# Performance work log

Hardware: AMD Instinct MI355X
Metric: run time of the kernel (lower is better)

Reference implementation:

```python
import jax, jax.numpy as jnp
import numpy as np
from jax import lax


def setup_inputs() -> dict:
    key = jax.random.key(0)
    k1, k2, k3 = jax.random.split(key, 3)
    H = W = 2048
    K, p = 16, 15
    x = jax.random.uniform(k1, (1, 1, H, W), dtype=jnp.float32)
    patterns = jax.random.uniform(k2, (K, p, p), dtype=jnp.float32)
    vectors = jax.random.normal(k3, (K, 2), dtype=jnp.float32)
    return {"x": x, "patterns": patterns, "vectors": vectors}


def reference(x, patterns, vectors):
    K, p, _ = patterns.shape
    img = x[0, 0]                      # [H, W]
    H, W = img.shape
    # GENEO_1: pad by p on all sides; window at (i,j) covers padded [i:i+p, j:j+p]
    padded = jnp.pad(img, p)           # [H+2p, W+2p]
    ones_k = jnp.ones((1, 1, p, p), dtype=img.dtype)
    win_sum = lax.conv_general_dilated(
        padded[None, None], ones_k, window_strides=(1, 1), padding='VALID'
    )[0, 0]                            # [H+p+1, W+p+1]
    win_sum = win_sum[:H, :W]          # windows for i in [0,H), j in [0,W)
    # out[k,i,j] = 1 - (sum(pattern_k) - win_sum)/(p*p)
    pat_sum = patterns.sum(axis=(1, 2))                     # [K]
    F_k = 1.0 - (pat_sum[:, None, None] - win_sum[None]) / (p * p)  # [K,H,W]
    # GENEO_3: gather at (i - floor(vx), j - floor(vy)), torch negative-index wrap -> mod
    off = jnp.floor(vectors).astype(jnp.int32)              # [K,2]
    ri = (jnp.arange(H)[None, :] - off[:, 0:1]) % H          # [K,H]
    rj = (jnp.arange(W)[None, :] - off[:, 1:2]) % W          # [K,W]
    gathered = F_k[jnp.arange(K)[:, None, None], ri[:, :, None], rj[:, None, :]]  # [K,H,W]
    # original divides by final loop variable k == K-1 (faithful)
    out = gathered.sum(axis=0) / (K - 1)
    return out
```

## Files before the change

### kernel.cpp

```cpp
#include <hip/hip_runtime.h>
#include <math.h>

#define H 2048
#define W 2048
#define K 16
#define P 15
#define CH 16
#define WP 2052

typedef float v4 __attribute__((ext_vector_type(4)));
typedef v4 uv4 __attribute__((aligned(4)));

__global__ void geneo_vpass(const float* __restrict__ img,
                            float* __restrict__ tmp) {
    int j  = (blockIdx.x * blockDim.x + threadIdx.x) * 4;
    int r0 = blockIdx.y * CH;
    v4 s = {0.f, 0.f, 0.f, 0.f};
    #pragma unroll
    for (int d = P; d >= 1; --d) {
        int a = r0 - d;
        if (a >= 0) s += *(const v4*)&img[a * W + j];
    }
    #pragma unroll
    for (int ii = 0; ii < CH; ++ii) {
        int i = r0 + ii;
        *(v4*)&tmp[i * W + j] = s;
        s += *(const v4*)&img[i * W + j];
        int rem = i - P;
        if (rem >= 0) s -= *(const v4*)&img[rem * W + j];
    }
}

__global__ void geneo_hpass(const float* __restrict__ tmp,
                            float* __restrict__ win) {
    __shared__ float lds[1040];
    int i  = blockIdx.y;
    int j0 = blockIdx.x * 1024;
    int t  = threadIdx.x;

    {
        int g = j0 - 16 + 4 * t;
        v4 v = (g >= 0) ? *(const v4*)&tmp[i * W + g] : (v4){0.f, 0.f, 0.f, 0.f};
        *(v4*)&lds[4 * t] = v;
        if (t < 4) {
            int g2 = j0 + 1008 + 4 * t;
            *(v4*)&lds[1024 + 4 * t] = *(const v4*)&tmp[i * W + g2];
        }
    }
    __syncthreads();

    int b = 4 * t + 1;
    float s0 = 0.f;
    #pragma unroll
    for (int m = 0; m < P; ++m) s0 += lds[b + m];
    float s1 = s0 - lds[b]     + lds[b + 15];
    float s2 = s1 - lds[b + 1] + lds[b + 16];
    float s3 = s2 - lds[b + 2] + lds[b + 17];
    v4 r = {s0, s1, s2, s3};
    *(v4*)&win[i * WP + j0 + 4 * t] = r;
    if (blockIdx.x == 0 && t == 0)
        *(v4*)&win[i * WP + W] = r;
}

__global__ void geneo_gather(const float* __restrict__ win,
                             const float* __restrict__ patterns,
                             const float* __restrict__ vectors,
                             float* __restrict__ out) {
    __shared__ float wsum[4];
    __shared__ int soy[K], sox[K];
    int t = threadIdx.x;

    float ps = 0.f;
    #pragma unroll
    for (int q = 0; q < 4; ++q) {
        int idx = t + q * 256;
        if (idx < 900) {
            v4 v = *(const v4*)&patterns[idx * 4];
            ps += (v.x + v.y) + (v.z + v.w);
        }
    }
    #pragma unroll
    for (int d = 32; d > 0; d >>= 1) ps += __shfl_down(ps, d, 64);
    if ((t & 63) == 0) wsum[t >> 6] = ps;
    if (t < K) {
        soy[t] = (int)floorf(vectors[2 * t]);
        sox[t] = (int)floorf(vectors[2 * t + 1]);
    }
    __syncthreads();

    float total = (wsum[0] + wsum[1]) + (wsum[2] + wsum[3]);
    const float invpp = 1.0f / 225.0f;
    float C = (16.0f - total * invpp) * (1.0f / 15.0f);
    const float S = invpp * (1.0f / 15.0f);

    int i = blockIdx.y;
    int j = (blockIdx.x * 256 + t) * 4;
    v4 acc = {0.f, 0.f, 0.f, 0.f};
    #pragma unroll
    for (int k = 0; k < K; ++k) {
        int ri = (i - soy[k]) & (H - 1);
        int rj = (j - sox[k]) & (W - 1);
        acc += *(const uv4*)&win[ri * WP + rj];
    }
    v4 o = acc * S + C;
    *(v4*)&out[i * W + j] = o;
}

extern "C" void kernel_launch(void* const* d_in, const int* in_sizes, int n_in,
                              void* d_out, int out_size, void* d_ws, size_t ws_size,
                              hipStream_t stream) {
    const float* x        = (const float*)d_in[0];
    const float* patterns = (const float*)d_in[1];
    const float* vectors  = (const float*)d_in[2];
    float* out = (float*)d_out;

    float* tmp = (float*)d_ws;
    float* win = tmp + H * W;

    geneo_vpass<<<dim3(2, H / CH), 256, 0, stream>>>(x, tmp);
    geneo_hpass<<<dim3(2, H), 256, 0, stream>>>(tmp, win);
    geneo_gather<<<dim3(2, H), 256, 0, stream>>>(win, patterns, vectors, out);
}
```

Before: 108.6 us.

## Fuse vertical and horizontal box-sum passes into one tiled LDS kernel

Merges the vertical column-sum pass and the horizontal row-sum pass into a single kernel. Each block computes column sums for a 32x256 tile into shared memory, then does the horizontal sliding sum from LDS. This removes the full-size intermediate buffer round-trip through global memory. The pattern-sum reduction and the offset flooring move into one block of that kernel and are handed to the gather kernel through the workspace. The gather grid is also remapped so that each XCD handles a contiguous band of rows, which is meant to improve L2 locality. The trade-offs are a block-0 serial prologue, scalar rather than vector loads in the column pass, and a halo recompute of 16 extra columns per tile.

New measurement: 114.2 us. +5.2%, slower.

```diff
diff --git a/kernel.cpp b/kernel.cpp
--- a/kernel.cpp
+++ b/kernel.cpp
@@ -5,96 +5,111 @@
 #define W 2048
 #define K 16
 #define P 15
-#define CH 16
 #define WP 2052
+#define LP 272
 
 typedef float v4 __attribute__((ext_vector_type(4)));
 typedef v4 uv4 __attribute__((aligned(4)));
 
-__global__ void geneo_vpass(const float* __restrict__ img,
-                            float* __restrict__ tmp) {
-    int j  = (blockIdx.x * blockDim.x + threadIdx.x) * 4;
-    int r0 = blockIdx.y * CH;
-    v4 s = {0.f, 0.f, 0.f, 0.f};
+__global__ void geneo_win(const float* __restrict__ img,
+                          float* __restrict__ win,
+                          const float* __restrict__ patterns,
+                          const float* __restrict__ vectors,
+                          float* __restrict__ consts,
+                          int* __restrict__ offs) {
+    __shared__ float cs[32][LP];
+    __shared__ float psum[4];
+    int t  = threadIdx.x;
+    int c0 = blockIdx.x * 256;
+    int r0 = blockIdx.y * 32;
+
+    if (blockIdx.x == 0 && blockIdx.y == 0) {
+        float ps = 0.f;
+        #pragma unroll
+        for (int q = 0; q < 4; ++q) {
+            int idx = t + q * 256;
+            if (idx < 900) {
+                v4 v = *(const v4*)&patterns[idx * 4];
+                ps += (v.x + v.y) + (v.z + v.w);
+            }
+        }
+        #pragma unroll
+        for (int d = 32; d > 0; d >>= 1) ps += __shfl_down(ps, d, 64);
+        if ((t & 63) == 0) psum[t >> 6] = ps;
+        if (t < 2 * K) offs[t] = (int)floorf(vectors[t]);
+        __syncthreads();
+        if (t == 0) {
+            float total = (psum[0] + psum[1]) + (psum[2] + psum[3]);
+            consts[0] = (16.0f - total * (1.0f / 225.0f)) * (1.0f / 15.0f);
+        }
+    }
+
+    int col0 = c0 - 16 + t;
+    int col1 = c0 + 240 + t;
+    bool ok0 = (col0 >= 0);
+    float s0 = 0.f, s1 = 0.f;
     #pragma unroll
-    for (int d = P; d >= 1; --d) {
-        int a = r0 - d;
-        if (a >= 0) s += *(const v4*)&img[a * W + j];
+    for (int d = 15; d >= 1; --d) {
+        int r = r0 - d;
+        if (r >= 0) {
+            if (ok0) s0 += img[r * W + col0];
+            if (t < 16) s1 += img[r * W + col1];
+        }
     }
     #pragma unroll
-    for (int ii = 0; ii < CH; ++ii) {
-        int i = r0 + ii;
-        *(v4*)&tmp[i * W + j] = s;
-        s += *(const v4*)&img[i * W + j];
-        int rem = i - P;
-        if (rem >= 0) s -= *(const v4*)&img[rem * W + j];
-    }
-}
-
-__global__ void geneo_hpass(const float* __restrict__ tmp,
-                            float* __restrict__ win) {
-    __shared__ float lds[1040];
-    int i  = blockIdx.y;
-    int j0 = blockIdx.x * 1024;
-    int t  = threadIdx.x;
-
-    {
-        int g = j0 - 16 + 4 * t;
-        v4 v = (g >= 0) ? *(const v4*)&tmp[i * W + g] : (v4){0.f, 0.f, 0.f, 0.f};
-        *(v4*)&lds[4 * t] = v;
-        if (t < 4) {
-            int g2 = j0 + 1008 + 4 * t;
-            *(v4*)&lds[1024 + 4 * t] = *(const v4*)&tmp[i * W + g2];
+    for (int ii = 0; ii < 32; ++ii) {
+        cs[ii][t] = s0;
+        if (t < 16) cs[ii][256 + t] = s1;
+        int r = r0 + ii;
+        if (ok0) s0 += img[r * W + col0];
+        if (t < 16) s1 += img[r * W + col1];
+        int rr = r - P;
+        if (rr >= 0) {
+            if (ok0) s0 -= img[rr * W + col0];
+            if (t < 16) s1 -= img[rr * W + col1];
         }
     }
     __syncthreads();
 
-    int b = 4 * t + 1;
-    float s0 = 0.f;
+    int cg = t & 63;
+    int rs = t >> 6;
+    int b  = 4 * cg + 1;
     #pragma unroll
-    for (int m = 0; m < P; ++m) s0 += lds[b + m];
-    float s1 = s0 - lds[b]     + lds[b + 15];
-    float s2 = s1 - lds[b + 1] + lds[b + 16];
-    float s3 = s2 - lds[b + 2] + lds[b + 17];
-    v4 r = {s0, s1, s2, s3};
-    *(v4*)&win[i * WP + j0 + 4 * t] = r;
-    if (blockIdx.x == 0 && t == 0)
-        *(v4*)&win[i * WP + W] = r;
+    for (int ib = 0; ib < 32; ib += 4) {
+        int ii = ib + rs;
+        const float* row = &cs[ii][0];
+        float x0 = 0.f;
+        #pragma unroll
+        for (int m = 0; m < P; ++m) x0 += row[b + m];
+        float x1 = x0 - row[b]     + row[b + 15];
+        float x2 = x1 - row[b + 1] + row[b + 16];
+        float x3 = x2 - row[b + 2] + row[b + 17];
+        v4 r4 = {x0, x1, x2, x3};
+        int gi = r0 + ii;
+        *(v4*)&win[gi * WP + c0 + 4 * cg] = r4;
+        if (blockIdx.x == 0 && cg == 0)
+            *(v4*)&win[gi * WP + W] = r4;
+    }
 }
 
 __global__ void geneo_gather(const float* __restrict__ win,
-                             const float* __restrict__ patterns,
-                             const float* __restrict__ vectors,
+                             const float* __restrict__ consts,
+                             const int* __restrict__ offs,
                              float* __restrict__ out) {
-    __shared__ float wsum[4];
     __shared__ int soy[K], sox[K];
+    __shared__ float sC;
     int t = threadIdx.x;
-
-    float ps = 0.f;
-    #pragma unroll
-    for (int q = 0; q < 4; ++q) {
-        int idx = t + q * 256;
-        if (idx < 900) {
-            v4 v = *(const v4*)&patterns[idx * 4];
-            ps += (v.x + v.y) + (v.z + v.w);
-        }
-    }
-    #pragma unroll
-    for (int d = 32; d > 0; d >>= 1) ps += __shfl_down(ps, d, 64);
-    if ((t & 63) == 0) wsum[t >> 6] = ps;
-    if (t < K) {
-        soy[t] = (int)floorf(vectors[2 * t]);
-        sox[t] = (int)floorf(vectors[2 * t + 1]);
-    }
+    if (t < K) { soy[t] = offs[t * 2]; sox[t] = offs[t * 2 + 1]; }
+    if (t == 0) sC = consts[0];
     __syncthreads();
 
-    float total = (wsum[0] + wsum[1]) + (wsum[2] + wsum[3]);
-    const float invpp = 1.0f / 225.0f;
-    float C = (16.0f - total * invpp) * (1.0f / 15.0f);
-    const float S = invpp * (1.0f / 15.0f);
+    int d   = blockIdx.x;
+    int xcd = d & 7;
+    int m   = d >> 3;
+    int i   = xcd * 256 + (m >> 1);
+    int j   = (m & 1) * 1024 + 4 * t;
 
-    int i = blockIdx.y;
-    int j = (blockIdx.x * 256 + t) * 4;
+    const float S = 1.0f / 3375.0f;
     v4 acc = {0.f, 0.f, 0.f, 0.f};
     #pragma unroll
     for (int k = 0; k < K; ++k) {
@@ -102,7 +117,7 @@
         int rj = (j - sox[k]) & (W - 1);
         acc += *(const uv4*)&win[ri * WP + rj];
     }
-    v4 o = acc * S + C;
+    v4 o = acc * S + sC;
     *(v4*)&out[i * W + j] = o;
 }
 
@@ -114,10 +129,10 @@
     const float* vectors  = (const float*)d_in[2];
     float* out = (float*)d_out;
 
-    float* tmp = (float*)d_ws;
-    float* win = tmp + H * W;
+    float* win    = (float*)d_ws;
+    float* consts = win + H * WP;
+    int*   offs   = (int*)(consts + 1);
 
-    geneo_vpass<<<dim3(2, H / CH), 256, 0, stream>>>(x, tmp);
-    geneo_hpass<<<dim3(2, H), 256, 0, stream>>>(tmp, win);
-    geneo_gather<<<dim3(2, H), 256, 0, stream>>>(win, patterns, vectors, out);
+    geneo_win<<<dim3(8, 64), 256, 0, stream>>>(x, win, patterns, vectors, consts, offs);
+    geneo_gather<<<4096, 256, 0, stream>>>(win, consts, offs, out);
 }
```
